# Performance work log

Measured on AMD Instinct MI355X. Metric: run time of the kernel, lower is better.

The kernel has to match this reference:

```python
import jax, jax.numpy as jnp
import numpy as np

HID, HEADS, LAYERS = 64, 4, 2
D = HID // HEADS
NU, NE, NV = 30000, 60000, 1000
N_NODES = (NU, NE, NV)
OFFS = (0, NU, NU + NE, NU + NE + NV)
N_TOTAL = NU + NE + NV
# (src_type, dst_type, n_edges); node types: user=0, event=1, venue=2. Order matches module.edge_types.
EDGE_DEFS = (
    (0, 0, 150000),  # friend
    (0, 1, 120000), (0, 1, 60000), (0, 1, 40000), (0, 1, 30000), (0, 1, 50000),  # view/like/save/intent/attend
    (1, 0, 120000), (1, 0, 60000), (1, 0, 40000), (1, 0, 30000), (1, 0, 50000),  # rev_*
    (1, 2, 60000),  # hosted_at
    (2, 1, 60000),  # hosts
)
EDGE_NAMES = ('ei_friend', 'ei_view', 'ei_like', 'ei_save', 'ei_intent', 'ei_attend',
              'ei_rev_view', 'ei_rev_like', 'ei_rev_save', 'ei_rev_intent', 'ei_rev_attend',
              'ei_hosted_at', 'ei_hosts')


def _l2norm(x):
    return x / jnp.maximum(jnp.linalg.norm(x, axis=-1, keepdims=True), 1e-12)


def _hgt_layer(h, edges, Wkqv, bkqv, Wk, Wv, p_rel, Wout, bout, skip):
    # h: list of per-node-type features [N_t, HID]. Fused K/Q/V projection per node type.
    kqv = [h[t] @ Wkqv[t] + bkqv[t] for t in range(3)]  # [N_t, 3*HID]
    k = [a[:, :HID].reshape(-1, HEADS, D) for a in kqv]
    q = [a[:, HID:2 * HID].reshape(-1, HEADS, D) for a in kqv]
    v = [a[:, 2 * HID:].reshape(-1, HEADS, D) for a in kqv]
    scale = 1.0 / np.sqrt(D).astype(np.float32)
    scores, msgs, dsts = [], [], []
    for e, (s, d, _) in enumerate(EDGE_DEFS):
        src_idx, dst_idx = edges[e][0], edges[e][1]
        # per-(edge_type, head) DxD relation transforms (PyG k_rel / v_rel)
        ke = jnp.einsum('nhd,hde->nhe', k[s], Wk[e])[src_idx]  # [E,H,D]
        ve = jnp.einsum('nhd,hde->nhe', v[s], Wv[e])[src_idx]  # [E,H,D]
        qi = q[d][dst_idx]                                      # [E,H,D]
        scores.append((qi * ke).sum(-1) * p_rel[e] * scale)     # [E,H]
        msgs.append(ve)
        dsts.append(dst_idx + OFFS[d])
    sc = jnp.concatenate(scores)   # [E_tot, H]
    ms = jnp.concatenate(msgs)     # [E_tot, H, D]
    dst = jnp.concatenate(dsts)    # [E_tot] global destination ids
    # destination-grouped softmax across all edge types jointly
    smax = jax.lax.stop_gradient(jax.ops.segment_max(sc, dst, num_segments=N_TOTAL))
    ex = jnp.exp(sc - smax[dst])
    den = jax.ops.segment_sum(ex, dst, num_segments=N_TOTAL)
    alpha = ex / den[dst]
    agg = jax.ops.segment_sum(alpha[:, :, None] * ms, dst, num_segments=N_TOTAL).reshape(N_TOTAL, HID)
    out = []
    for t in range(3):
        o = agg[OFFS[t]:OFFS[t + 1]]
        a = jax.nn.gelu(o, approximate=False) @ Wout[t] + bout[t]
        g = jax.nn.sigmoid(skip[t])  # learnable skip gate
        out.append(g * a + (1.0 - g) * h[t])
    return out


def _forward(x_user, x_event, x_venue, W_user, b_user, W_event, b_event, W_venue, b_venue,
             emb_user, emb_event, emb_venue, Wkqv, bkqv, Wk, Wv, p_rel, Wout, bout, skip,
             ids_user, ids_event, ids_venue, edges):
    h = [x_user @ W_user + b_user + emb_user[ids_user],
         x_event @ W_event + b_event + emb_event[ids_event],
         x_venue @ W_venue + b_venue + emb_venue[ids_venue]]
    for l in range(LAYERS):
        h = _hgt_layer(h, edges, Wkqv[l], bkqv[l], Wk[l], Wv[l], p_rel[l], Wout[l], bout[l], skip[l])
        h = [jax.nn.relu(x) for x in h]  # dropout is identity in eval mode
    return tuple(_l2norm(x) for x in h)


def setup_inputs() -> dict:
    key = jax.random.key(0)
    ks = iter(jax.random.split(key, 64))
    s = 0.05
    inp = {
        'x_user': jax.random.normal(next(ks), (NU, 32), jnp.float32),
        'x_event': jax.random.normal(next(ks), (NE, 32), jnp.float32),
        'x_venue': jax.random.normal(next(ks), (NV, 16), jnp.float32),
        'W_user': jax.random.normal(next(ks), (32, HID), jnp.float32) * s,
        'b_user': jnp.zeros((HID,), jnp.float32),
        'W_event': jax.random.normal(next(ks), (32, HID), jnp.float32) * s,
        'b_event': jnp.zeros((HID,), jnp.float32),
        'W_venue': jax.random.normal(next(ks), (16, HID), jnp.float32) * s,
        'b_venue': jnp.zeros((HID,), jnp.float32),
        'emb_user': jax.random.normal(next(ks), (NU, HID), jnp.float32) * s,
        'emb_event': jax.random.normal(next(ks), (NE, HID), jnp.float32) * s,
        'emb_venue': jax.random.normal(next(ks), (NV, HID), jnp.float32) * s,
        'Wkqv': jax.random.normal(next(ks), (LAYERS, 3, HID, 3 * HID), jnp.float32) * s,
        'bkqv': jnp.zeros((LAYERS, 3, 3 * HID), jnp.float32),
        'Wk': jax.random.normal(next(ks), (LAYERS, 13, HEADS, D, D), jnp.float32) * 0.2,
        'Wv': jax.random.normal(next(ks), (LAYERS, 13, HEADS, D, D), jnp.float32) * 0.2,
        'p_rel': jnp.ones((LAYERS, 13, HEADS), jnp.float32),
        'Wout': jax.random.normal(next(ks), (LAYERS, 3, HID, HID), jnp.float32) * s,
        'bout': jnp.zeros((LAYERS, 3, HID), jnp.float32),
        'skip': jnp.ones((LAYERS, 3), jnp.float32),
        'ids_user': jnp.arange(NU, dtype=jnp.int32),
        'ids_event': jnp.arange(NE, dtype=jnp.int32),
        'ids_venue': jnp.arange(NV, dtype=jnp.int32),
    }
    for name, (st, dt, n) in zip(EDGE_NAMES, EDGE_DEFS):
        src = jax.random.randint(next(ks), (n,), 0, N_NODES[st], dtype=jnp.int32)
        dst = jax.random.randint(next(ks), (n,), 0, N_NODES[dt], dtype=jnp.int32)
        inp[name] = jnp.stack([src, dst])
    return inp


def reference(x_user, x_event, x_venue, W_user, b_user, W_event, b_event, W_venue, b_venue,
              emb_user, emb_event, emb_venue, Wkqv, bkqv, Wk, Wv, p_rel, Wout, bout, skip,
              ids_user, ids_event, ids_venue,
              ei_friend, ei_view, ei_like, ei_save, ei_intent, ei_attend,
              ei_rev_view, ei_rev_like, ei_rev_save, ei_rev_intent, ei_rev_attend,
              ei_hosted_at, ei_hosts):
    edges = (ei_friend, ei_view, ei_like, ei_save, ei_intent, ei_attend,
             ei_rev_view, ei_rev_like, ei_rev_save, ei_rev_intent, ei_rev_attend,
             ei_hosted_at, ei_hosts)
    return _forward(x_user, x_event, x_venue, W_user, b_user, W_event, b_event, W_venue, b_venue,
                    emb_user, emb_event, emb_venue, Wkqv, bkqv, Wk, Wv, p_rel, Wout, bout, skip,
                    ids_user, ids_event, ids_venue, edges)
```

## Files before the change

### kernel.cpp

```cpp
#include <hip/hip_runtime.h>
#include <hip/hip_fp16.h>
#include <math.h>

#define HID   64
#define HEADS 4
#define DH    16
#define NU    30000
#define NE_   60000
#define NV    1000
#define NTOT  91000
#define ETOT  870000
#define NSLOT 541000
#define LAYERS 2

__device__ const int d_EOFF[14] = {0,150000,270000,330000,370000,400000,450000,
                                   570000,630000,670000,700000,750000,810000,870000};
__device__ const int d_ECNT[13] = {150000,120000,60000,40000,30000,50000,
                                   120000,60000,40000,30000,50000,60000,60000};
__device__ const int d_EST[13]  = {0,0,0,0,0,0,1,1,1,1,1,1,2};
__device__ const int d_EDT[13]  = {0,1,1,1,1,1,0,0,0,0,0,2,1};
__device__ const int d_NOFF[3]  = {0, NU, NU + NE_};
__device__ const int d_EBASE[13] = {0,30000,60000,90000,120000,150000,
                                    180000,240000,300000,360000,420000,480000,540000};

struct EdgePtrs { const int* p[13]; };

typedef float f32x2 __attribute__((ext_vector_type(2)));

__device__ __forceinline__ void pk_fma(f32x2& acc, f32x2 a, f32x2 b) {
    asm("v_pk_fma_f32 %0, %1, %2, %0" : "+v"(acc) : "v"(a), "v"(b));
}
__device__ __forceinline__ void pk_fma_sv(f32x2& acc, f32x2 a_sgpr, f32x2 b) {
    asm("v_pk_fma_f32 %0, %1, %2, %0" : "+v"(acc) : "s"(a_sgpr), "v"(b));
}

__device__ __forceinline__ int node_type(int n) {
    return (n >= NU) + (n >= NU + NE_);
}

__global__ __launch_bounds__(64)
void k_init(const float* __restrict__ xu, const float* __restrict__ xe,
            const float* __restrict__ xv,
            const float* __restrict__ Wu, const float* __restrict__ bu,
            const float* __restrict__ We, const float* __restrict__ be,
            const float* __restrict__ Wv_, const float* __restrict__ bv,
            const float* __restrict__ embu, const float* __restrict__ embe,
            const float* __restrict__ embv,
            const int* __restrict__ idu, const int* __restrict__ ide,
            const int* __restrict__ idv,
            float* __restrict__ h) {
    int n0 = blockIdx.x * 16;
    int t = node_type(n0);
    int j = threadIdx.x;
    const float *x, *W, *bb, *emb; const int* ids; int in_dim;
    if (t == 0)      { x = xu; W = Wu;  bb = bu; emb = embu; ids = idu; in_dim = 32; }
    else if (t == 1) { x = xe; W = We;  bb = be; emb = embe; ids = ide; in_dim = 32; }
    else             { x = xv; W = Wv_; bb = bv; emb = embv; ids = idv; in_dim = 16; }
    int nl = n0 - d_NOFF[t];
    int nn = min(16, NTOT - n0);
    __shared__ float xT[32][20];
    int ncs = (in_dim == 32) ? 3 : 2;
    int nch = 1 << ncs;
    for (int idx = j; idx < (nch << 4); idx += 64) {
        int n = idx >> ncs, c = idx & (nch - 1);
        float4 v = make_float4(0.f, 0.f, 0.f, 0.f);
        if (n < nn) v = *(const float4*)(x + (size_t)(nl + n) * in_dim + c * 4);
        xT[c * 4 + 0][n] = v.x;
        xT[c * 4 + 1][n] = v.y;
        xT[c * 4 + 2][n] = v.z;
        xT[c * 4 + 3][n] = v.w;
    }
    __syncthreads();
    float bj = bb[j];
    f32x2 acc2[8];
    #pragma unroll
    for (int p = 0; p < 8; p++) {
        float ex = (2 * p     < nn) ? emb[(size_t)ids[nl + 2 * p    ] * 64 + j] : 0.f;
        float ey = (2 * p + 1 < nn) ? emb[(size_t)ids[nl + 2 * p + 1] * 64 + j] : 0.f;
        acc2[p].x = bj + ex; acc2[p].y = bj + ey;
    }
    if (in_dim == 32) {
        #pragma unroll
        for (int i = 0; i < 32; i++) {
            float w = W[i * 64 + j];
            f32x2 w2; w2.x = w; w2.y = w;
            #pragma unroll
            for (int qd = 0; qd < 4; qd++) {
                float4 hv = *(const float4*)(&xT[i][qd * 4]);
                f32x2 p0; p0.x = hv.x; p0.y = hv.y; pk_fma(acc2[2 * qd],     p0, w2);
                f32x2 p1; p1.x = hv.z; p1.y = hv.w; pk_fma(acc2[2 * qd + 1], p1, w2);
            }
        }
    } else {
        #pragma unroll
        for (int i = 0; i < 16; i++) {
            float w = W[i * 64 + j];
            f32x2 w2; w2.x = w; w2.y = w;
            #pragma unroll
            for (int qd = 0; qd < 4; qd++) {
                float4 hv = *(const float4*)(&xT[i][qd * 4]);
                f32x2 p0; p0.x = hv.x; p0.y = hv.y; pk_fma(acc2[2 * qd],     p0, w2);
                f32x2 p1; p1.x = hv.z; p1.y = hv.w; pk_fma(acc2[2 * qd + 1], p1, w2);
            }
        }
    }
    #pragma unroll
    for (int p = 0; p < 8; p++) {
        if (2 * p     < nn) h[(size_t)(n0 + 2 * p)     * 64 + j] = acc2[p].x;
        if (2 * p + 1 < nn) h[(size_t)(n0 + 2 * p + 1) * 64 + j] = acc2[p].y;
    }
}

__global__ void k_cnt(EdgePtrs ep, int* __restrict__ cnt) {
    int eidx = blockIdx.x * blockDim.x + threadIdx.x;
    if (eidx >= ETOT) return;
    int e = 0;
    #pragma unroll
    for (int i = 1; i < 13; i++) e += (eidx >= d_EOFF[i]);
    int li = eidx - d_EOFF[e];
    int dst = ep.p[e][d_ECNT[e] + li];
    atomicAdd(&cnt[d_NOFF[d_EDT[e]] + dst], 1);
}

__global__ void k_scan_a(const int* __restrict__ cnt, int* __restrict__ partial) {
    __shared__ int s[256];
    int i = blockIdx.x * 256 + threadIdx.x;
    s[threadIdx.x] = (i < NTOT) ? cnt[i] : 0;
    __syncthreads();
    for (int off = 128; off > 0; off >>= 1) {
        if (threadIdx.x < off) s[threadIdx.x] += s[threadIdx.x + off];
        __syncthreads();
    }
    if (threadIdx.x == 0) partial[blockIdx.x] = s[0];
}

__global__ void k_scan_b(int* __restrict__ partial, int nblk) {
    __shared__ int s[512];
    int t = threadIdx.x;
    s[t] = (t < nblk) ? partial[t] : 0;
    __syncthreads();
    for (int off = 1; off < 512; off <<= 1) {
        int v = (t >= off) ? s[t - off] : 0;
        __syncthreads();
        s[t] += v;
        __syncthreads();
    }
    if (t < nblk) partial[t] = t ? s[t - 1] : 0;
}

__global__ void k_scan_c(const int* __restrict__ cnt, const int* __restrict__ partial,
                         int* __restrict__ row_ptr) {
    __shared__ int s[256];
    int i = blockIdx.x * 256 + threadIdx.x, t = threadIdx.x;
    int v = (i < NTOT) ? cnt[i] : 0;
    s[t] = v;
    __syncthreads();
    for (int off = 1; off < 256; off <<= 1) {
        int u = (t >= off) ? s[t - off] : 0;
        __syncthreads();
        s[t] += u;
        __syncthreads();
    }
    if (i < NTOT) row_ptr[i] = s[t] - v + partial[blockIdx.x];
    if (i == NTOT - 1) row_ptr[NTOT] = s[t] + partial[blockIdx.x];
}

__global__ void k_fill(EdgePtrs ep, const int* __restrict__ row_ptr,
                       int* __restrict__ cursor, int* __restrict__ csr) {
    int eidx = blockIdx.x * blockDim.x + threadIdx.x;
    if (eidx >= ETOT) return;
    int e = 0;
    #pragma unroll
    for (int i = 1; i < 13; i++) e += (eidx >= d_EOFF[i]);
    int li = eidx - d_EOFF[e];
    const int* base = ep.p[e];
    int src = base[li], dst = base[d_ECNT[e] + li];
    int dg = d_NOFF[d_EDT[e]] + dst;
    int pos = atomicAdd(&cursor[dg], 1);
    csr[row_ptr[dg] + pos] = d_EBASE[e] + src;
}

__global__ __launch_bounds__(192, 3)
void k_kqvt(const float* __restrict__ h, const float* __restrict__ Wkqv,
            const float* __restrict__ bkqv, const float* __restrict__ Wk,
            const float* __restrict__ Wv, const float* __restrict__ prel,
            float* __restrict__ qagg, __half2* __restrict__ kvt, int layer) {
    int n0 = blockIdx.x * 16;
    int t = node_type(n0);
    __shared__ float kq[16][192];
    int j = threadIdx.x;

    const float* hb = h + (size_t)n0 * 64;
    const float* Wc = Wkqv + (size_t)(layer * 3 + t) * HID * 192 + j;
    float b = bkqv[(layer * 3 + t) * 192 + j];
    f32x2 acc2[16];
    #pragma unroll
    for (int n = 0; n < 16; n++) { acc2[n].x = 0.f; acc2[n].y = 0.f; }
    #pragma unroll
    for (int ic = 0; ic < 16; ic++) {
        float w0 = Wc[(size_t)(4 * ic + 0) * 192];
        float w1 = Wc[(size_t)(4 * ic + 1) * 192];
        float w2 = Wc[(size_t)(4 * ic + 2) * 192];
        float w3 = Wc[(size_t)(4 * ic + 3) * 192];
        f32x2 wA; wA.x = w0; wA.y = w1;
        f32x2 wB; wB.x = w2; wB.y = w3;
        #pragma unroll
        for (int n = 0; n < 16; n++) {
            float4 hv = *(const float4*)(hb + n * 64 + ic * 4);
            f32x2 p0; p0.x = hv.x; p0.y = hv.y;
            pk_fma_sv(acc2[n], p0, wA);
            f32x2 p1; p1.x = hv.z; p1.y = hv.w;
            pk_fma_sv(acc2[n], p1, wB);
        }
    }
    float accf[16];
    #pragma unroll
    for (int n = 0; n < 16; n++) accf[n] = b + acc2[n].x + acc2[n].y;
    #pragma unroll
    for (int n = 0; n < 16; n++) kq[n][j] = accf[n];
    if (j >= 64 && j < 128) {
        #pragma unroll
        for (int n = 0; n < 16; n++)
            if (n0 + n < NTOT) qagg[(size_t)(n0 + n) * 64 + (j - 64)] = accf[n];
    }
    __syncthreads();

    int wave = j >> 6, lane = j & 63;
    int hh = lane >> 4, xo = lane & 15;
    int ne = (t == 2) ? 1 : 6;
    int e0 = (t == 0) ? 0 : (t == 1) ? 6 : 12;
    int eA = e0 + wave, eB = e0 + wave + 3;
    bool vA = wave < ne, vB = wave + 3 < ne;
    int nt = n0 - d_NOFF[t];
    f32x2 wkA[8], wvA[8], wkB[8], wvB[8];
    int sbA = 0, sbB = 0;
    if (vA) {
        const float* Wkp = Wk + (((size_t)layer * 13 + eA) * 4 + hh) * 256 + xo;
        const float* Wvp = Wv + (((size_t)layer * 13 + eA) * 4 + hh) * 256 + xo;
        float pr = prel[(layer * 13 + eA) * 4 + hh] * 0.25f;
        #pragma unroll
        for (int p = 0; p < 8; p++) {
            wkA[p].x = Wkp[(2 * p)     * 16] * pr;
            wkA[p].y = Wkp[(2 * p + 1) * 16] * pr;
            wvA[p].x = Wvp[(2 * p)     * 16];
            wvA[p].y = Wvp[(2 * p + 1) * 16];
        }
        sbA = d_EBASE[eA] + nt;
    }
    if (vB) {
        const float* Wkp = Wk + (((size_t)layer * 13 + eB) * 4 + hh) * 256 + xo;
        const float* Wvp = Wv + (((size_t)layer * 13 + eB) * 4 + hh) * 256 + xo;
        float pr = prel[(layer * 13 + eB) * 4 + hh] * 0.25f;
        #pragma unroll
        for (int p = 0; p < 8; p++) {
            wkB[p].x = Wkp[(2 * p)     * 16] * pr;
            wkB[p].y = Wkp[(2 * p + 1) * 16] * pr;
            wvB[p].x = Wvp[(2 * p)     * 16];
            wvB[p].y = Wvp[(2 * p + 1) * 16];
        }
        sbB = d_EBASE[eB] + nt;
    }
    #pragma unroll
    for (int n = 0; n < 16; n++) {
        bool ok = (n0 + n) < NTOT;
        const float* kr = &kq[n][hh * 16];
        const float* vr = &kq[n][128 + hh * 16];
        float4 k0 = ((const float4*)kr)[0];
        float4 k1 = ((const float4*)kr)[1];
        float4 k2 = ((const float4*)kr)[2];
        float4 k3 = ((const float4*)kr)[3];
        float4 v0 = ((const float4*)vr)[0];
        float4 v1 = ((const float4*)vr)[1];
        float4 v2 = ((const float4*)vr)[2];
        float4 v3 = ((const float4*)vr)[3];
        if (vA & ok) {
            f32x2 ak; ak.x = 0.f; ak.y = 0.f;
            f32x2 av; av.x = 0.f; av.y = 0.f;
            f32x2 p0;
            p0.x = k0.x; p0.y = k0.y; pk_fma(ak, p0, wkA[0]);
            p0.x = k0.z; p0.y = k0.w; pk_fma(ak, p0, wkA[1]);
            p0.x = k1.x; p0.y = k1.y; pk_fma(ak, p0, wkA[2]);
            p0.x = k1.z; p0.y = k1.w; pk_fma(ak, p0, wkA[3]);
            p0.x = k2.x; p0.y = k2.y; pk_fma(ak, p0, wkA[4]);
            p0.x = k2.z; p0.y = k2.w; pk_fma(ak, p0, wkA[5]);
            p0.x = k3.x; p0.y = k3.y; pk_fma(ak, p0, wkA[6]);
            p0.x = k3.z; p0.y = k3.w; pk_fma(ak, p0, wkA[7]);
            p0.x = v0.x; p0.y = v0.y; pk_fma(av, p0, wvA[0]);
            p0.x = v0.z; p0.y = v0.w; pk_fma(av, p0, wvA[1]);
            p0.x = v1.x; p0.y = v1.y; pk_fma(av, p0, wvA[2]);
            p0.x = v1.z; p0.y = v1.w; pk_fma(av, p0, wvA[3]);
            p0.x = v2.x; p0.y = v2.y; pk_fma(av, p0, wvA[4]);
            p0.x = v2.z; p0.y = v2.w; pk_fma(av, p0, wvA[5]);
            p0.x = v3.x; p0.y = v3.y; pk_fma(av, p0, wvA[6]);
            p0.x = v3.z; p0.y = v3.w; pk_fma(av, p0, wvA[7]);
            float kt = ak.x + ak.y;
            float vt = av.x + av.y;
            kvt[(size_t)(sbA + n) * 64 + lane] = __float22half2_rn(make_float2(kt, vt));
        }
        if (vB & ok) {
            f32x2 ak; ak.x = 0.f; ak.y = 0.f;
            f32x2 av; av.x = 0.f; av.y = 0.f;
            f32x2 p0;
            p0.x = k0.x; p0.y = k0.y; pk_fma(ak, p0, wkB[0]);
            p0.x = k0.z; p0.y = k0.w; pk_fma(ak, p0, wkB[1]);
            p0.x = k1.x; p0.y = k1.y; pk_fma(ak, p0, wkB[2]);
            p0.x = k1.z; p0.y = k1.w; pk_fma(ak, p0, wkB[3]);
            p0.x = k2.x; p0.y = k2.y; pk_fma(ak, p0, wkB[4]);
            p0.x = k2.z; p0.y = k2.w; pk_fma(ak, p0, wkB[5]);
            p0.x = k3.x; p0.y = k3.y; pk_fma(ak, p0, wkB[6]);
            p0.x = k3.z; p0.y = k3.w; pk_fma(ak, p0, wkB[7]);
            p0.x = v0.x; p0.y = v0.y; pk_fma(av, p0, wvB[0]);
            p0.x = v0.z; p0.y = v0.w; pk_fma(av, p0, wvB[1]);
            p0.x = v1.x; p0.y = v1.y; pk_fma(av, p0, wvB[2]);
            p0.x = v1.z; p0.y = v1.w; pk_fma(av, p0, wvB[3]);
            p0.x = v2.x; p0.y = v2.y; pk_fma(av, p0, wvB[4]);
            p0.x = v2.z; p0.y = v2.w; pk_fma(av, p0, wvB[5]);
            p0.x = v3.x; p0.y = v3.y; pk_fma(av, p0, wvB[6]);
            p0.x = v3.z; p0.y = v3.w; pk_fma(av, p0, wvB[7]);
            float kt = ak.x + ak.y;
            float vt = av.x + av.y;
            kvt[(size_t)(sbB + n) * 64 + lane] = __float22half2_rn(make_float2(kt, vt));
        }
    }
}

__device__ __forceinline__ float row_sum16(float x) {
    int v;
    v = __builtin_amdgcn_update_dpp(0, __float_as_int(x), 0xB1, 0xF, 0xF, true);
    x += __int_as_float(v);
    v = __builtin_amdgcn_update_dpp(0, __float_as_int(x), 0x4E, 0xF, 0xF, true);
    x += __int_as_float(v);
    v = __builtin_amdgcn_update_dpp(0, __float_as_int(x), 0x141, 0xF, 0xF, true);
    x += __int_as_float(v);
    v = __builtin_amdgcn_update_dpp(0, __float_as_int(x), 0x140, 0xF, 0xF, true);
    x += __int_as_float(v);
    return x;
}

__device__ __forceinline__ void osm_step(float s, float vv,
                                         float& m, float& l, float& acc) {
    float d = s - m;
    float t = __expf(-fabsf(d));
    bool pos = d > 0.f;
    m = fmaxf(m, s);
    float sc = pos ? t : 1.f;
    float es = pos ? 1.f : t;
    l   = l * sc + es;
    acc = acc * sc + es * vv;
}

__global__ __launch_bounds__(512, 8)
void k_gather(float* __restrict__ qagg, const __half2* __restrict__ kvt,
              const int* __restrict__ row_ptr, const int* __restrict__ csr) {
    int wave = threadIdx.x >> 6, lane = threadIdx.x & 63;
    int node = blockIdx.x * 8 + wave;
    if (node >= NTOT) return;
    float q = qagg[(size_t)node * 64 + lane];
    int beg = row_ptr[node], end = row_ptr[node + 1];
    float m0 = -1e30f, l0 = 0.f, a0 = 0.f;
    float m1 = -1e30f, l1 = 0.f, a1 = 0.f;
    for (int base = beg; base < end; base += 64) {
        int n = end - base; if (n > 64) n = 64;
        int ent = csr[base + ((lane < n) ? lane : 0)];
        for (int c = 0; c < n; c += 8) {
            int cn = n - c; if (cn > 8) cn = 8;
            __half2 f[8];
            #pragma unroll
            for (int k = 0; k < 8; k++) {
                int idx = c + ((k < cn) ? k : 0);
                int sl = __shfl(ent, idx, 64);
                f[k] = kvt[(size_t)sl * 64 + lane];
            }
            float s8[8];
            #pragma unroll
            for (int k = 0; k < 8; k++) {
                if (k >= cn) break;
                s8[k] = row_sum16(q * __low2float(f[k]));
            }
            #pragma unroll
            for (int k = 0; k < 8; k += 2) {
                if (k < cn)     osm_step(s8[k],   __high2float(f[k]),   m0, l0, a0);
                if (k + 1 < cn) osm_step(s8[k+1], __high2float(f[k+1]), m1, l1, a1);
            }
        }
    }
    float M   = fmaxf(m0, m1);
    float e0  = __expf(m0 - M), e1 = __expf(m1 - M);
    float l   = l0 * e0 + l1 * e1;
    float acc = a0 * e0 + a1 * e1;
    qagg[(size_t)node * 64 + lane] = (l > 0.f) ? acc / l : 0.f;
}

__global__ __launch_bounds__(256)
void k_out(const float* __restrict__ agg, const float* __restrict__ Wout,
           const float* __restrict__ bout, const float* __restrict__ skip,
           float* __restrict__ h, float* __restrict__ out, int layer, int last) {
    int b = blockIdx.x; int t, n0, lim;
    if (b < 938)       { t = 0; n0 = b * 32;                 lim = NU; }
    else if (b < 2813) { t = 1; n0 = NU + (b - 938) * 32;    lim = NU + NE_; }
    else               { t = 2; n0 = NU + NE_ + (b - 2813) * 32; lim = NTOT; }
    int nn = min(32, lim - n0);
    __shared__ float gsT[64][36];
    for (int i = threadIdx.x; i < nn * 64; i += 256) {
        float o = agg[(size_t)n0 * 64 + i];
        gsT[i & 63][i >> 6] = 0.5f * o * (1.f + erff(o * 0.70710678118654752f));
    }
    __syncthreads();
    int j = threadIdx.x & 63, g = threadIdx.x >> 6;
    const float* W = Wout + (size_t)(layer * 3 + t) * HID * HID;
    float bb = bout[(layer * 3 + t) * HID + j];
    f32x2 acc2[4];
    #pragma unroll
    for (int p = 0; p < 4; p++) { acc2[p].x = bb; acc2[p].y = bb; }
    for (int i = 0; i < 64; i++) {
        float w = W[i * 64 + j];
        f32x2 w2; w2.x = w; w2.y = w;
        float4 a = *(const float4*)(&gsT[i][g * 8]);
        float4 c = *(const float4*)(&gsT[i][g * 8 + 4]);
        f32x2 p0; p0.x = a.x; p0.y = a.y; pk_fma(acc2[0], p0, w2);
        f32x2 p1; p1.x = a.z; p1.y = a.w; pk_fma(acc2[1], p1, w2);
        f32x2 p2; p2.x = c.x; p2.y = c.y; pk_fma(acc2[2], p2, w2);
        f32x2 p3; p3.x = c.z; p3.y = c.w; pk_fma(acc2[3], p3, w2);
    }
    float acc[8];
    #pragma unroll
    for (int p = 0; p < 4; p++) { acc[2 * p] = acc2[p].x; acc[2 * p + 1] = acc2[p].y; }
    float gk = 1.f / (1.f + __expf(-skip[layer * 3 + t]));
    #pragma unroll
    for (int n = 0; n < 8; n++) {
        int node = n0 + g * 8 + n;
        if (node >= lim) continue;
        float r = gk * acc[n] + (1.f - gk) * h[(size_t)node * 64 + j];
        r = fmaxf(r, 0.f);
        if (!last) {
            h[(size_t)node * 64 + j] = r;
        } else {
            float ss = r * r;
            ss += __shfl_xor(ss, 1, 64);  ss += __shfl_xor(ss, 2, 64);
            ss += __shfl_xor(ss, 4, 64);  ss += __shfl_xor(ss, 8, 64);
            ss += __shfl_xor(ss, 16, 64); ss += __shfl_xor(ss, 32, 64);
            float nrm = fmaxf(sqrtf(ss), 1e-12f);
            out[(size_t)node * 64 + j] = r / nrm;
        }
    }
}

extern "C" void kernel_launch(void* const* d_in, const int* in_sizes, int n_in,
                              void* d_out, int out_size, void* d_ws, size_t ws_size,
                              hipStream_t stream) {
    const float* xu   = (const float*)d_in[0];
    const float* xe   = (const float*)d_in[1];
    const float* xv   = (const float*)d_in[2];
    const float* Wu   = (const float*)d_in[3];
    const float* bu   = (const float*)d_in[4];
    const float* We   = (const float*)d_in[5];
    const float* be   = (const float*)d_in[6];
    const float* Wv_  = (const float*)d_in[7];
    const float* bv   = (const float*)d_in[8];
    const float* embu = (const float*)d_in[9];
    const float* embe = (const float*)d_in[10];
    const float* embv = (const float*)d_in[11];
    const float* Wkqv = (const float*)d_in[12];
    const float* bkqv = (const float*)d_in[13];
    const float* Wk   = (const float*)d_in[14];
    const float* Wv   = (const float*)d_in[15];
    const float* prel = (const float*)d_in[16];
    const float* Wout = (const float*)d_in[17];
    const float* bout = (const float*)d_in[18];
    const float* skip = (const float*)d_in[19];
    const int*   idu  = (const int*)d_in[20];
    const int*   ide  = (const int*)d_in[21];
    const int*   idv  = (const int*)d_in[22];
    EdgePtrs ep;
    for (int e = 0; e < 13; e++) ep.p[e] = (const int*)d_in[23 + e];

    float* ws  = (float*)d_ws;
    float* h      = ws;
    float* qagg   = h    + (size_t)NTOT * HID;
    __half2* kvt  = (__half2*)(qagg + (size_t)NTOT * HID);
    int* cnt     = (int*)(kvt + (size_t)NSLOT * HID);
    int* cursor  = cnt + NTOT;
    int* row_ptr = cursor + NTOT;
    int* partial = row_ptr + NTOT + 1;
    int* csr     = partial + 512;

    k_init<<<(NTOT + 15) / 16, 64, 0, stream>>>(
        xu, xe, xv, Wu, bu, We, be, Wv_, bv, embu, embe, embv, idu, ide, idv, h);

    hipMemsetAsync(cnt, 0, (size_t)2 * NTOT * 4, stream);
    int nblk = (NTOT + 255) / 256;
    k_cnt<<<(ETOT + 255) / 256, 256, 0, stream>>>(ep, cnt);
    k_scan_a<<<nblk, 256, 0, stream>>>(cnt, partial);
    k_scan_b<<<1, 512, 0, stream>>>(partial, nblk);
    k_scan_c<<<nblk, 256, 0, stream>>>(cnt, partial, row_ptr);
    k_fill<<<(ETOT + 255) / 256, 256, 0, stream>>>(ep, row_ptr, cursor, csr);

    for (int l = 0; l < LAYERS; l++) {
        k_kqvt<<<(NTOT + 15) / 16, 192, 0, stream>>>(h, Wkqv, bkqv, Wk, Wv, prel,
                                                     qagg, kvt, l);
        k_gather<<<(NTOT + 7) / 8, 512, 0, stream>>>(qagg, kvt, row_ptr, csr);
        k_out<<<2845, 256, 0, stream>>>(qagg, Wout, bout, skip, h,
                                        (float*)d_out, l, l == LAYERS - 1);
    }
}
```

Before: 623.7 us.

## Precompose KQV projection with per-relation K/V transforms into fused weight matrix

Adds a k_fuse kernel that multiplies the per-type K and V projection columns by each edge type's relation matrices (scaled by p_rel/sqrt(D)) and writes one concatenated weight and bias table per layer. k_kqvt then computes q and every relation-transformed k/v directly from h in a single GEMM-like pass, with no shared-memory staging and no second small matmul. This drops the intermediate stage and its sync, but each node now does 64x(64+768) FMAs instead of 64x192 plus the small transforms. It also uses 512-thread blocks with up to 448 active threads, adds a launch, and changes float rounding order.

```diff
diff --git a/kernel.cpp b/kernel.cpp
--- a/kernel.cpp
+++ b/kernel.cpp
@@ -12,6 +12,7 @@
 #define ETOT  870000
 #define NSLOT 541000
 #define LAYERS 2
+#define NCOLS 1856
 
 __device__ const int d_EOFF[14] = {0,150000,270000,330000,370000,400000,450000,
                                    570000,630000,670000,700000,750000,810000,870000};
@@ -180,147 +181,120 @@
     csr[row_ptr[dg] + pos] = d_EBASE[e] + src;
 }
 
-__global__ __launch_bounds__(192, 3)
-void k_kqvt(const float* __restrict__ h, const float* __restrict__ Wkqv,
-            const float* __restrict__ bkqv, const float* __restrict__ Wk,
-            const float* __restrict__ Wv, const float* __restrict__ prel,
+__global__ __launch_bounds__(64)
+void k_fuse(const float* __restrict__ Wkqv, const float* __restrict__ bkqv,
+            const float* __restrict__ Wk, const float* __restrict__ Wv,
+            const float* __restrict__ prel,
+            float* __restrict__ Wcat, float* __restrict__ bcat) {
+    int blk = blockIdx.x;
+    int l = blk / NCOLS, c = blk % NCOLS;
+    int t = (c < 832) ? 0 : (c < 1664) ? 1 : 2;
+    int tc = c - ((t == 0) ? 0 : (t == 1) ? 832 : 1664);
+    int i = threadIdx.x;
+    const float* Wsrc = Wkqv + (size_t)(l * 3 + t) * 64 * 192;
+    const float* bsrc = bkqv + (l * 3 + t) * 192;
+    float wval, bval = 0.f;
+    if (tc < 64) {
+        wval = Wsrc[i * 192 + 64 + tc];
+        bval = bsrc[64 + tc];
+    } else {
+        int idx = tc - 64, el = idx >> 7, r = idx & 127;
+        int isv = r >> 6, lcol = r & 63, hh = lcol >> 4, xo = lcol & 15;
+        int e0 = (t == 0) ? 0 : (t == 1) ? 6 : 12;
+        int e = e0 + el;
+        const float* M = (isv ? Wv : Wk) + (((size_t)(l * 13 + e)) * 4 + hh) * 256 + xo;
+        float pr = isv ? 1.f : prel[(l * 13 + e) * 4 + hh] * 0.25f;
+        int kc = (isv ? 128 : 0) + hh * 16;
+        float s = 0.f;
+        #pragma unroll
+        for (int d = 0; d < 16; d++) s += Wsrc[i * 192 + kc + d] * M[d * 16];
+        wval = s * pr;
+        if (i == 0) {
+            float sb = 0.f;
+            #pragma unroll
+            for (int d = 0; d < 16; d++) sb += bsrc[kc + d] * M[d * 16];
+            bval = sb * pr;
+        }
+    }
+    Wcat[((size_t)l * NCOLS + c) * 64 + i] = wval;
+    if (i == 0) bcat[l * NCOLS + c] = bval;
+}
+
+__global__ __launch_bounds__(512)
+void k_kqvt(const float* __restrict__ h, const float* __restrict__ Wcat,
+            const float* __restrict__ bcat,
             float* __restrict__ qagg, __half2* __restrict__ kvt, int layer) {
     int n0 = blockIdx.x * 16;
     int t = node_type(n0);
-    __shared__ float kq[16][192];
-    int j = threadIdx.x;
-
+    int U = (t == 2) ? 128 : 448;
+    int u = threadIdx.x;
+    if (u >= U) return;
+    int nn = min(16, NTOT - n0);
     const float* hb = h + (size_t)n0 * 64;
-    const float* Wc = Wkqv + (size_t)(layer * 3 + t) * HID * 192 + j;
-    float b = bkqv[(layer * 3 + t) * 192 + j];
-    f32x2 acc2[16];
-    #pragma unroll
-    for (int n = 0; n < 16; n++) { acc2[n].x = 0.f; acc2[n].y = 0.f; }
-    #pragma unroll
-    for (int ic = 0; ic < 16; ic++) {
-        float w0 = Wc[(size_t)(4 * ic + 0) * 192];
-        float w1 = Wc[(size_t)(4 * ic + 1) * 192];
-        float w2 = Wc[(size_t)(4 * ic + 2) * 192];
-        float w3 = Wc[(size_t)(4 * ic + 3) * 192];
-        f32x2 wA; wA.x = w0; wA.y = w1;
-        f32x2 wB; wB.x = w2; wB.y = w3;
+    int coff = (t == 0) ? 0 : (t == 1) ? 832 : 1664;
+    size_t lbase = (size_t)layer * NCOLS;
+
+    if (u < 64) {
+        const float* Wq = Wcat + (lbase + coff + u) * 64;
+        float bq = bcat[lbase + coff + u];
+        f32x2 acc[16];
+        #pragma unroll
+        for (int n = 0; n < 16; n++) { acc[n].x = bq; acc[n].y = 0.f; }
+        #pragma unroll
+        for (int ic = 0; ic < 16; ic++) {
+            float4 w4 = *(const float4*)(Wq + ic * 4);
+            f32x2 wA; wA.x = w4.x; wA.y = w4.y;
+            f32x2 wB; wB.x = w4.z; wB.y = w4.w;
+            #pragma unroll
+            for (int n = 0; n < 16; n++) {
+                float4 hv = *(const float4*)(hb + n * 64 + ic * 4);
+                f32x2 p0; p0.x = hv.x; p0.y = hv.y; pk_fma_sv(acc[n], p0, wA);
+                f32x2 p1; p1.x = hv.z; p1.y = hv.w; pk_fma_sv(acc[n], p1, wB);
+            }
+        }
+        #pragma unroll
+        for (int n = 0; n < 16; n++)
+            if (n < nn) qagg[(size_t)(n0 + n) * 64 + u] = acc[n].x + acc[n].y;
+    } else {
+        int idx = u - 64, el = idx >> 6, lcol = idx & 63;
+        int e0 = (t == 0) ? 0 : (t == 1) ? 6 : 12;
+        int e = e0 + el;
+        int ckt = coff + 64 + el * 128 + lcol;
+        const float* Wkt = Wcat + (lbase + ckt) * 64;
+        const float* Wvt = Wkt + 64 * 64;
+        float bk = bcat[lbase + ckt], bv = bcat[lbase + ckt + 64];
+        f32x2 ak[16], av[16];
         #pragma unroll
         for (int n = 0; n < 16; n++) {
-            float4 hv = *(const float4*)(hb + n * 64 + ic * 4);
-            f32x2 p0; p0.x = hv.x; p0.y = hv.y;
-            pk_fma_sv(acc2[n], p0, wA);
-            f32x2 p1; p1.x = hv.z; p1.y = hv.w;
-            pk_fma_sv(acc2[n], p1, wB);
-        }
-    }
-    float accf[16];
-    #pragma unroll
-    for (int n = 0; n < 16; n++) accf[n] = b + acc2[n].x + acc2[n].y;
-    #pragma unroll
-    for (int n = 0; n < 16; n++) kq[n][j] = accf[n];
-    if (j >= 64 && j < 128) {
+            ak[n].x = bk; ak[n].y = 0.f;
+            av[n].x = bv; av[n].y = 0.f;
+        }
+        #pragma unroll
+        for (int ic = 0; ic < 16; ic++) {
+            float4 wk4 = *(const float4*)(Wkt + ic * 4);
+            float4 wv4 = *(const float4*)(Wvt + ic * 4);
+            f32x2 kA; kA.x = wk4.x; kA.y = wk4.y;
+            f32x2 kB; kB.x = wk4.z; kB.y = wk4.w;
+            f32x2 vA; vA.x = wv4.x; vA.y = wv4.y;
+            f32x2 vB; vB.x = wv4.z; vB.y = wv4.w;
+            #pragma unroll
+            for (int n = 0; n < 16; n++) {
+                float4 hv = *(const float4*)(hb + n * 64 + ic * 4);
+                f32x2 p0; p0.x = hv.x; p0.y = hv.y;
+                f32x2 p1; p1.x = hv.z; p1.y = hv.w;
+                pk_fma_sv(ak[n], p0, kA);
+                pk_fma_sv(ak[n], p1, kB);
+                pk_fma_sv(av[n], p0, vA);
+                pk_fma_sv(av[n], p1, vB);
+            }
+        }
+        int sb = d_EBASE[e] + (n0 - d_NOFF[t]);
         #pragma unroll
         for (int n = 0; n < 16; n++)
-            if (n0 + n < NTOT) qagg[(size_t)(n0 + n) * 64 + (j - 64)] = accf[n];
-    }
-    __syncthreads();
-
-    int wave = j >> 6, lane = j & 63;
-    int hh = lane >> 4, xo = lane & 15;
-    int ne = (t == 2) ? 1 : 6;
-    int e0 = (t == 0) ? 0 : (t == 1) ? 6 : 12;
-    int eA = e0 + wave, eB = e0 + wave + 3;
-    bool vA = wave < ne, vB = wave + 3 < ne;
-    int nt = n0 - d_NOFF[t];
-    f32x2 wkA[8], wvA[8], wkB[8], wvB[8];
-    int sbA = 0, sbB = 0;
-    if (vA) {
-        const float* Wkp = Wk + (((size_t)layer * 13 + eA) * 4 + hh) * 256 + xo;
-        const float* Wvp = Wv + (((size_t)layer * 13 + eA) * 4 + hh) * 256 + xo;
-        float pr = prel[(layer * 13 + eA) * 4 + hh] * 0.25f;
-        #pragma unroll
-        for (int p = 0; p < 8; p++) {
-            wkA[p].x = Wkp[(2 * p)     * 16] * pr;
-            wkA[p].y = Wkp[(2 * p + 1) * 16] * pr;
-            wvA[p].x = Wvp[(2 * p)     * 16];
-            wvA[p].y = Wvp[(2 * p + 1) * 16];
-        }
-        sbA = d_EBASE[eA] + nt;
-    }
-    if (vB) {
-        const float* Wkp = Wk + (((size_t)layer * 13 + eB) * 4 + hh) * 256 + xo;
-        const float* Wvp = Wv + (((size_t)layer * 13 + eB) * 4 + hh) * 256 + xo;
-        float pr = prel[(layer * 13 + eB) * 4 + hh] * 0.25f;
-        #pragma unroll
-        for (int p = 0; p < 8; p++) {
-            wkB[p].x = Wkp[(2 * p)     * 16] * pr;
-            wkB[p].y = Wkp[(2 * p + 1) * 16] * pr;
-            wvB[p].x = Wvp[(2 * p)     * 16];
-            wvB[p].y = Wvp[(2 * p + 1) * 16];
-        }
-        sbB = d_EBASE[eB] + nt;
-    }
-    #pragma unroll
-    for (int n = 0; n < 16; n++) {
-        bool ok = (n0 + n) < NTOT;
-        const float* kr = &kq[n][hh * 16];
-        const float* vr = &kq[n][128 + hh * 16];
-        float4 k0 = ((const float4*)kr)[0];
-        float4 k1 = ((const float4*)kr)[1];
-        float4 k2 = ((const float4*)kr)[2];
-        float4 k3 = ((const float4*)kr)[3];
-        float4 v0 = ((const float4*)vr)[0];
-        float4 v1 = ((const float4*)vr)[1];
-        float4 v2 = ((const float4*)vr)[2];
-        float4 v3 = ((const float4*)vr)[3];
-        if (vA & ok) {
-            f32x2 ak; ak.x = 0.f; ak.y = 0.f;
-            f32x2 av; av.x = 0.f; av.y = 0.f;
-            f32x2 p0;
-            p0.x = k0.x; p0.y = k0.y; pk_fma(ak, p0, wkA[0]);
-            p0.x = k0.z; p0.y = k0.w; pk_fma(ak, p0, wkA[1]);
-            p0.x = k1.x; p0.y = k1.y; pk_fma(ak, p0, wkA[2]);
-            p0.x = k1.z; p0.y = k1.w; pk_fma(ak, p0, wkA[3]);
-            p0.x = k2.x; p0.y = k2.y; pk_fma(ak, p0, wkA[4]);
-            p0.x = k2.z; p0.y = k2.w; pk_fma(ak, p0, wkA[5]);
-            p0.x = k3.x; p0.y = k3.y; pk_fma(ak, p0, wkA[6]);
-            p0.x = k3.z; p0.y = k3.w; pk_fma(ak, p0, wkA[7]);
-            p0.x = v0.x; p0.y = v0.y; pk_fma(av, p0, wvA[0]);
-            p0.x = v0.z; p0.y = v0.w; pk_fma(av, p0, wvA[1]);
-            p0.x = v1.x; p0.y = v1.y; pk_fma(av, p0, wvA[2]);
-            p0.x = v1.z; p0.y = v1.w; pk_fma(av, p0, wvA[3]);
-            p0.x = v2.x; p0.y = v2.y; pk_fma(av, p0, wvA[4]);
-            p0.x = v2.z; p0.y = v2.w; pk_fma(av, p0, wvA[5]);
-            p0.x = v3.x; p0.y = v3.y; pk_fma(av, p0, wvA[6]);
-            p0.x = v3.z; p0.y = v3.w; pk_fma(av, p0, wvA[7]);
-            float kt = ak.x + ak.y;
-            float vt = av.x + av.y;
-            kvt[(size_t)(sbA + n) * 64 + lane] = __float22half2_rn(make_float2(kt, vt));
-        }
-        if (vB & ok) {
-            f32x2 ak; ak.x = 0.f; ak.y = 0.f;
-            f32x2 av; av.x = 0.f; av.y = 0.f;
-            f32x2 p0;
-            p0.x = k0.x; p0.y = k0.y; pk_fma(ak, p0, wkB[0]);
-            p0.x = k0.z; p0.y = k0.w; pk_fma(ak, p0, wkB[1]);
-            p0.x = k1.x; p0.y = k1.y; pk_fma(ak, p0, wkB[2]);
-            p0.x = k1.z; p0.y = k1.w; pk_fma(ak, p0, wkB[3]);
-            p0.x = k2.x; p0.y = k2.y; pk_fma(ak, p0, wkB[4]);
-            p0.x = k2.z; p0.y = k2.w; pk_fma(ak, p0, wkB[5]);
-            p0.x = k3.x; p0.y = k3.y; pk_fma(ak, p0, wkB[6]);
-            p0.x = k3.z; p0.y = k3.w; pk_fma(ak, p0, wkB[7]);
-            p0.x = v0.x; p0.y = v0.y; pk_fma(av, p0, wvB[0]);
-            p0.x = v0.z; p0.y = v0.w; pk_fma(av, p0, wvB[1]);
-            p0.x = v1.x; p0.y = v1.y; pk_fma(av, p0, wvB[2]);
-            p0.x = v1.z; p0.y = v1.w; pk_fma(av, p0, wvB[3]);
-            p0.x = v2.x; p0.y = v2.y; pk_fma(av, p0, wvB[4]);
-            p0.x = v2.z; p0.y = v2.w; pk_fma(av, p0, wvB[5]);
-            p0.x = v3.x; p0.y = v3.y; pk_fma(av, p0, wvB[6]);
-            p0.x = v3.z; p0.y = v3.w; pk_fma(av, p0, wvB[7]);
-            float kt = ak.x + ak.y;
-            float vt = av.x + av.y;
-            kvt[(size_t)(sbB + n) * 64 + lane] = __float22half2_rn(make_float2(kt, vt));
-        }
+            if (n < nn)
+                kvt[(size_t)(sb + n) * 64 + lcol] =
+                    __float22half2_rn(make_float2(ak[n].x + ak[n].y,
+                                                  av[n].x + av[n].y));
     }
 }
 
@@ -483,9 +457,13 @@
     int* row_ptr = cursor + NTOT;
     int* partial = row_ptr + NTOT + 1;
     int* csr     = partial + 512;
+    float* Wcat  = (float*)(csr + ETOT);
+    float* bcat  = Wcat + (size_t)2 * NCOLS * 64;
 
     k_init<<<(NTOT + 15) / 16, 64, 0, stream>>>(
         xu, xe, xv, Wu, bu, We, be, Wv_, bv, embu, embe, embv, idu, ide, idv, h);
+
+    k_fuse<<<2 * NCOLS, 64, 0, stream>>>(Wkqv, bkqv, Wk, Wv, prel, Wcat, bcat);
 
     hipMemsetAsync(cnt, 0, (size_t)2 * NTOT * 4, stream);
     int nblk = (NTOT + 255) / 256;
@@ -496,8 +474,7 @@
     k_fill<<<(ETOT + 255) / 256, 256, 0, stream>>>(ep, row_ptr, cursor, csr);
 
     for (int l = 0; l < LAYERS; l++) {
-        k_kqvt<<<(NTOT + 15) / 16, 192, 0, stream>>>(h, Wkqv, bkqv, Wk, Wv, prel,
-                                                     qagg, kvt, l);
+        k_kqvt<<<(NTOT + 15) / 16, 512, 0, stream>>>(h, Wcat, bcat, qagg, kvt, l);
         k_gather<<<(NTOT + 7) / 8, 512, 0, stream>>>(qagg, kvt, row_ptr, csr);
         k_out<<<2845, 256, 0, stream>>>(qagg, Wout, bout, skip, h,
                                         (float*)d_out, l, l == LAYERS - 1);
```

Result: slower. 935.8 us (+50.0%).
